# Kernel tuning notes

Hardware: AMD Instinct MI355X
Metric: run time of the kernel (lower is better)

Reference implementation:

```python
import jax, jax.numpy as jnp
import numpy as np

LN_EPS = 1e-6

def _log_g(x):
    return jnp.where(x >= 0, jnp.log(jax.nn.relu(x) + 0.5), -jax.nn.softplus(-x))

def setup_inputs() -> dict:
    key = jax.random.key(0)
    k1, k2 = jax.random.split(key)
    B, T, D = 8, 4096, 1024
    x = jax.random.normal(k1, (B, T, D), dtype=jnp.float32)
    W = jax.random.normal(k2, (D, 2 * D), dtype=jnp.float32) * (1.0 / np.sqrt(D))
    b = jnp.zeros((2 * D,), dtype=jnp.float32)
    gamma = jnp.ones((D,), dtype=jnp.float32)
    beta = jnp.zeros((D,), dtype=jnp.float32)
    return {"x": x, "W": W, "b": b, "gamma": gamma, "beta": beta}

def reference(x, W, b, gamma, beta):
    # projection: [B,T,D] @ [D,2D] -> [B,T,2D]
    projected = jnp.einsum('btd,de->bte', x, W) + b
    h_tilde, k = jnp.split(projected, 2, axis=-1)
    log_coeffs = -jax.nn.softplus(k)          # log(1-z)
    log_z = -jax.nn.softplus(-k)               # log(z)
    log_values = log_z + _log_g(h_tilde)
    # parallel scan in log space along time axis (-2)
    a_star = jnp.cumsum(log_coeffs, axis=-2)
    log_h0_plus_b_star = jax.lax.associative_scan(jnp.logaddexp, log_values - a_star, axis=-2)
    h = jnp.exp(a_star + log_h0_plus_b_star)
    # residual + LayerNorm (eps = flax nnx default 1e-6)
    y = x + h
    mu = jnp.mean(y, axis=-1, keepdims=True)
    var = jnp.mean(jnp.square(y - mu), axis=-1, keepdims=True)
    return (y - mu) * jax.lax.rsqrt(var + LN_EPS) * gamma + beta
```

## Files before the change

### kernel.cpp

```cpp
#include <hip/hip_runtime.h>
#include <hip/hip_bf16.h>

#define B_  8
#define T_  4096
#define D_  1024
#define M_  (B_*T_)
#define N_  (2*D_)
#define K_  D_
#define NC_ 32
#define C_  (T_/NC_)

typedef short bf16x8 __attribute__((ext_vector_type(8)));
typedef float f32x4  __attribute__((ext_vector_type(4)));

__device__ __forceinline__ unsigned short f2bf(float f) {
  union { float f; unsigned int u; } v; v.f = f;
  unsigned int r = (v.u + 0x7fffu + ((v.u >> 16) & 1u)) >> 16;
  return (unsigned short)r;
}

__device__ __forceinline__ float bf2f(unsigned short u) {
  union { unsigned int u; float f; } v; v.u = ((unsigned int)u) << 16; return v.f;
}

__device__ __forceinline__ float sigm(float x) {
  return 1.0f / (1.0f + __expf(-x));
}

__device__ __forceinline__ void async16(const void* g, void* l) {
  __builtin_amdgcn_global_load_lds((const __attribute__((address_space(1))) void*)g,
                                   (__attribute__((address_space(3))) void*)l,
                                   16, 0, 0);
}

__global__ void cast_x_kernel(const float* __restrict__ x, unsigned short* __restrict__ xb) {
  const long n4 = (long)M_ * K_ / 4;
  long i = (long)blockIdx.x * blockDim.x + threadIdx.x;
  const long stride = (long)gridDim.x * blockDim.x;
  for (; i < n4; i += stride) {
    float4 v = ((const float4*)x)[i];
    ushort4 o;
    o.x = f2bf(v.x); o.y = f2bf(v.y); o.z = f2bf(v.z); o.w = f2bf(v.w);
    ((ushort4*)xb)[i] = o;
  }
}

__global__ void cast_wt_kernel(const float* __restrict__ W, unsigned short* __restrict__ Wt) {
  __shared__ float tile[32][33];
  const int n0 = blockIdx.x * 32, k0 = blockIdx.y * 32;
  const int tx = threadIdx.x, ty = threadIdx.y;
  for (int i = 0; i < 32; i += 8)
    tile[ty + i][tx] = W[(size_t)(k0 + ty + i) * N_ + n0 + tx];
  __syncthreads();
  for (int i = 0; i < 32; i += 8)
    Wt[(size_t)(n0 + ty + i) * K_ + k0 + tx] = f2bf(tile[tx][ty + i]);
}

#define BM 128
#define BN 128
#define BK 64

__global__ __launch_bounds__(256, 3) void gemm_kernel(
    const unsigned short* __restrict__ A,
    const unsigned short* __restrict__ Bt,
    const float* __restrict__ bias,
    unsigned short* __restrict__ Sout,
    unsigned short* __restrict__ Gout) {
  __shared__ unsigned short lds[2 * BM * BK];
  unsigned short* As = lds;
  unsigned short* Bs = lds + BM * BK;

  const int tid  = threadIdx.x;
  const int wave = tid >> 6;
  const int lane = tid & 63;

  const int bid   = blockIdx.x;
  const int xcd   = bid & 7;
  const int j     = bid >> 3;
  const int n_idx = j & 15;
  const int m_idx = (j >> 4) * 8 + xcd;
  const int m0 = m_idx * BM;
  const int n0 = n_idx * BN;

  const int wm = wave >> 1;
  const int wn = wave & 1;
  const int n15  = lane & 15;
  const int quad = lane >> 4;

  f32x4 acc[4][4] = {};

  for (int k0 = 0; k0 < K_; k0 += BK) {
    for (int i = 0; i < 4; ++i) {
      const int seg = wave * 4 + i;
      const int row = seg * 8 + (lane >> 3);
      const int gg  = ((lane & 7) ^ (row & 7)) * 8;
      async16(A  + (size_t)(m0 + row) * K_ + k0 + gg, As + seg * 512);
      async16(Bt + (size_t)(n0 + row) * K_ + k0 + gg, Bs + seg * 512);
    }
    __syncthreads();

    for (int kk = 0; kk < 2; ++kk) {
      const int gg = kk * 4 + quad;
      bf16x8 af[4], bfr[4];
      for (int i = 0; i < 4; ++i) {
        const int row = wm * 64 + i * 16 + n15;
        af[i] = *(const bf16x8*)(As + (size_t)row * BK + ((gg ^ (row & 7)) * 8));
      }
      for (int jj = 0; jj < 4; ++jj) {
        const int row = wn * 64 + jj * 16 + n15;
        bfr[jj] = *(const bf16x8*)(Bs + (size_t)row * BK + ((gg ^ (row & 7)) * 8));
      }
      for (int i = 0; i < 4; ++i)
        for (int jj = 0; jj < 4; ++jj)
          acc[i][jj] = __builtin_amdgcn_mfma_f32_16x16x32_bf16(af[i], bfr[jj], acc[i][jj], 0, 0, 0);
    }
    __syncthreads();
  }

  const bool is_k = (n0 >= D_);
  unsigned short* __restrict__ dst = is_k ? Sout : Gout;
  for (int jj = 0; jj < 4; ++jj) {
    const int n = n0 + wn * 64 + jj * 16 + n15;
    const float bv = bias[n];
    const int d = is_k ? (n - D_) : n;
    for (int i = 0; i < 4; ++i) {
      const int mbase = m0 + wm * 64 + i * 16 + quad * 4;
      for (int r = 0; r < 4; ++r) {
        const float val = acc[i][jj][r] + bv;
        float o;
        if (is_k) o = sigm(val);
        else      o = (val >= 0.0f) ? (val + 0.5f) : sigm(val);
        dst[(size_t)(mbase + r) * D_ + d] = f2bf(o);
      }
    }
  }
}

__global__ void chunk_agg_kernel(const unsigned short* __restrict__ S,
                                 const unsigned short* __restrict__ G,
                                 float* __restrict__ AggA, float* __restrict__ AggV) {
  const int d = blockIdx.x * 256 + threadIdx.x;
  const int c = blockIdx.y;
  const int b = blockIdx.z;
  size_t base = ((size_t)b * T_ + (size_t)c * C_) * D_ + d;
  float Aa = 1.0f, V = 0.0f;
  for (int t = 0; t < C_; ++t) {
    const float s = bf2f(S[base]);
    const float g = bf2f(G[base]);
    const float a = 1.0f - s;
    V = fmaf(a, V, s * g);
    Aa *= a;
    base += D_;
  }
  const int idx = (b * NC_ + c) * D_ + d;
  AggA[idx] = Aa;
  AggV[idx] = V;
}

__global__ void chunk_scan_kernel(const float* __restrict__ AggA, const float* __restrict__ AggV,
                                  float* __restrict__ H0) {
  const int d = blockIdx.x * 256 + threadIdx.x;
  const int b = blockIdx.y;
  float h = 0.0f;
  for (int c = 0; c < NC_; ++c) {
    const int idx = (b * NC_ + c) * D_ + d;
    H0[idx] = h;
    h = fmaf(AggA[idx], h, AggV[idx]);
  }
}

__global__ __launch_bounds__(1024, 1) void scan_ln_kernel(
    const unsigned short* __restrict__ S, const unsigned short* __restrict__ G,
    const float* __restrict__ x, const float* __restrict__ H0,
    const float* __restrict__ gamma, const float* __restrict__ beta,
    float* __restrict__ out) {
  __shared__ float yb[16 * 1024];
  const int d = threadIdx.x;
  const int c = blockIdx.x;
  const int b = blockIdx.y;
  const int wid = d >> 6, lane = d & 63;

  float h = H0[(b * NC_ + c) * D_ + d];
  float gam[16], bet[16];
  for (int j = 0; j < 16; ++j) { gam[j] = gamma[lane + 64 * j]; bet[j] = beta[lane + 64 * j]; }

  size_t base = ((size_t)b * T_ + (size_t)c * C_) * D_ + d;
  for (int batch = 0; batch < 8; ++batch) {
    for (int tt = 0; tt < 16; ++tt) {
      const size_t idx = base + (size_t)tt * D_;
      const float s = bf2f(S[idx]);
      const float g = bf2f(G[idx]);
      h = fmaf(s, g - h, h);
      yb[tt * 1024 + d] = x[idx] + h;
    }
    __syncthreads();
    {
      float sy = 0.0f, sq = 0.0f;
      float yv[16];
      for (int j = 0; j < 16; ++j) {
        const float v = yb[wid * 1024 + lane + 64 * j];
        yv[j] = v; sy += v; sq += v * v;
      }
      for (int o = 32; o > 0; o >>= 1) {
        sy += __shfl_down(sy, o);
        sq += __shfl_down(sq, o);
      }
      sy = __shfl(sy, 0); sq = __shfl(sq, 0);
      const float mu   = sy * (1.0f / D_);
      const float rstd = rsqrtf(sq * (1.0f / D_) - mu * mu + 1e-6f);
      const size_t obase = ((size_t)b * T_ + (size_t)c * C_ + (size_t)batch * 16 + wid) * D_;
      for (int j = 0; j < 16; ++j)
        out[obase + lane + 64 * j] = (yv[j] - mu) * rstd * gam[j] + bet[j];
    }
    __syncthreads();
    base += (size_t)16 * D_;
  }
}

extern "C" void kernel_launch(void* const* d_in, const int* in_sizes, int n_in,
                              void* d_out, int out_size, void* d_ws, size_t ws_size,
                              hipStream_t stream) {
  const float* x     = (const float*)d_in[0];
  const float* W     = (const float*)d_in[1];
  const float* bias  = (const float*)d_in[2];
  const float* gamma = (const float*)d_in[3];
  const float* beta  = (const float*)d_in[4];
  float* out = (float*)d_out;

  char* ws = (char*)d_ws;
  unsigned short* Wt = (unsigned short*)ws;  ws += (size_t)N_ * K_ * 2;
  unsigned short* Xb = (unsigned short*)ws;  ws += (size_t)M_ * K_ * 2;
  unsigned short* S  = (unsigned short*)ws;  ws += (size_t)M_ * D_ * 2;
  unsigned short* G  = (unsigned short*)ws;  ws += (size_t)M_ * D_ * 2;
  float* AggA = (float*)ws;                  ws += (size_t)B_ * NC_ * D_ * 4;
  float* AggV = (float*)ws;                  ws += (size_t)B_ * NC_ * D_ * 4;
  float* H0   = (float*)ws;                  ws += (size_t)B_ * NC_ * D_ * 4;

  cast_x_kernel<<<4096, 256, 0, stream>>>(x, Xb);
  cast_wt_kernel<<<dim3(N_ / 32, K_ / 32), dim3(32, 8), 0, stream>>>(W, Wt);
  gemm_kernel<<<4096, 256, 0, stream>>>(Xb, Wt, bias, S, G);
  chunk_agg_kernel<<<dim3(D_ / 256, NC_, B_), 256, 0, stream>>>(S, G, AggA, AggV);
  chunk_scan_kernel<<<dim3(D_ / 256, B_), 256, 0, stream>>>(AggA, AggV, H0);
  scan_ln_kernel<<<dim3(NC_, B_), 1024, 0, stream>>>(S, G, x, H0, gamma, beta, out);
}
```

Measured before the change: 474.3 us.

## Rewrite GEMM as 256x256 double-buffered pipeline with LDS-staged coalesced epilogue

The projection GEMM moves from 128x128 tiles with a synchronous load-then-compute loop to 256x256 tiles on 512 threads. Global-to-LDS async loads for the next K tile are interleaved with MFMA phases using explicit barriers, waitcnt and setprio. The epilogue writes activated bf16 results into swizzled LDS and then stores them as coalesced 16-byte rows instead of scattered 2-byte stores. The larger tiles improve data reuse and the overlap hides load latency, at the cost of more registers and 128KB of LDS per block, which limits occupancy.

```diff
diff --git a/kernel.cpp b/kernel.cpp
--- a/kernel.cpp
+++ b/kernel.cpp
@@ -56,83 +56,166 @@
     Wt[(size_t)(n0 + ty + i) * K_ + k0 + tx] = f2bf(tile[tx][ty + i]);
 }
 
-#define BM 128
-#define BN 128
+#define BM 256
+#define BN 256
 #define BK 64
-
-__global__ __launch_bounds__(256, 3) void gemm_kernel(
+#define NT (K_/BK)
+#define LDSA(b) ((b)*32768)
+#define LDSB(b) ((b)*32768 + 16384)
+
+#define BARX()  __builtin_amdgcn_s_barrier()
+#define LGKM0() asm volatile("s_waitcnt lgkmcnt(0)" ::: "memory")
+#define SB0()   __builtin_amdgcn_sched_barrier(0)
+#define VM8()   asm volatile("s_waitcnt vmcnt(8)" ::: "memory")
+#define VM0()   asm volatile("s_waitcnt vmcnt(0)" ::: "memory")
+
+#define STAGE_Bt(BUF, KOFF) do {                                                \
+    _Pragma("unroll")                                                           \
+    for (int r = 0; r < 4; ++r)                                                 \
+      async16(aB + (KOFF) + r*64*K_, lds + LDSB(BUF) + w*512 + r*4096);         \
+  } while (0)
+#define STAGE_At(BUF, KOFF) do {                                                \
+    _Pragma("unroll")                                                           \
+    for (int r = 0; r < 4; ++r)                                                 \
+      async16(aA + (KOFF) + r*64*K_, lds + LDSA(BUF) + w*512 + r*4096);         \
+  } while (0)
+
+#define RD_A(MBASE, BUF) do {                                                   \
+    _Pragma("unroll")                                                           \
+    for (int m = 0; m < 4; ++m) {                                               \
+      af[m][0] = *(const bf16x8*)(lds + LDSA(BUF) + (rowA + (MBASE + m)*16)*64 + cc0); \
+      af[m][1] = *(const bf16x8*)(lds + LDSA(BUF) + (rowA + (MBASE + m)*16)*64 + cc1); \
+    } } while (0)
+#define RD_B(NBASE, BUF) do {                                                   \
+    _Pragma("unroll")                                                           \
+    for (int n = 0; n < 2; ++n) {                                               \
+      bfr[NBASE + n][0] = *(const bf16x8*)(lds + LDSB(BUF) + (rowB + (NBASE + n)*16)*64 + cc0); \
+      bfr[NBASE + n][1] = *(const bf16x8*)(lds + LDSB(BUF) + (rowB + (NBASE + n)*16)*64 + cc1); \
+    } } while (0)
+
+#define MFMA_Q(MB, NB) do {                                                     \
+    __builtin_amdgcn_s_setprio(1);                                              \
+    _Pragma("unroll")                                                           \
+    for (int m = 0; m < 4; ++m)                                                 \
+      _Pragma("unroll")                                                         \
+      for (int n = 0; n < 2; ++n) {                                             \
+        acc[MB+m][NB+n] = __builtin_amdgcn_mfma_f32_16x16x32_bf16(af[m][0], bfr[NB+n][0], acc[MB+m][NB+n], 0, 0, 0); \
+        acc[MB+m][NB+n] = __builtin_amdgcn_mfma_f32_16x16x32_bf16(af[m][1], bfr[NB+n][1], acc[MB+m][NB+n], 0, 0, 0); \
+      }                                                                         \
+    __builtin_amdgcn_s_setprio(0);                                              \
+  } while (0)
+
+#define TILE(BUF, DO_STAGE, KOFF, VMW) do {                                     \
+                                                                        \
+    RD_A(0, BUF); RD_B(0, BUF);                                                 \
+    BARX(); LGKM0(); SB0();                                                     \
+    MFMA_Q(0, 0);                                                               \
+    BARX();                                                                     \
+                                                                        \
+    RD_B(2, BUF);                                                               \
+    BARX(); LGKM0(); SB0();                                                     \
+    MFMA_Q(0, 2);                                                               \
+    BARX();                                                                     \
+                                                                        \
+    if (DO_STAGE) STAGE_Bt(BUF, KOFF);                                          \
+    RD_A(4, BUF);                                                               \
+    BARX(); LGKM0(); SB0();                                                     \
+    MFMA_Q(4, 0);                                                               \
+    BARX();                                                                     \
+                                                                        \
+    if (DO_STAGE) STAGE_At(BUF, KOFF);                                          \
+    MFMA_Q(4, 2);                                                               \
+    VMW;                                                                        \
+    BARX();                                                                     \
+  } while (0)
+
+__global__ __launch_bounds__(512, 2) void gemm_kernel(
     const unsigned short* __restrict__ A,
     const unsigned short* __restrict__ Bt,
     const float* __restrict__ bias,
     unsigned short* __restrict__ Sout,
     unsigned short* __restrict__ Gout) {
-  __shared__ unsigned short lds[2 * BM * BK];
-  unsigned short* As = lds;
-  unsigned short* Bs = lds + BM * BK;
+  __shared__ unsigned short lds[65536];
 
   const int tid  = threadIdx.x;
-  const int wave = tid >> 6;
+  const int w    = tid >> 6;
   const int lane = tid & 63;
+  const int wm   = w >> 2;
+  const int wn   = w & 3;
+  const int quad = lane >> 4, n15 = lane & 15;
 
   const int bid   = blockIdx.x;
   const int xcd   = bid & 7;
   const int j     = bid >> 3;
-  const int n_idx = j & 15;
-  const int m_idx = (j >> 4) * 8 + xcd;
-  const int m0 = m_idx * BM;
-  const int n0 = n_idx * BN;
-
-  const int wm = wave >> 1;
-  const int wn = wave & 1;
-  const int n15  = lane & 15;
-  const int quad = lane >> 4;
-
-  f32x4 acc[4][4] = {};
-
-  for (int k0 = 0; k0 < K_; k0 += BK) {
-    for (int i = 0; i < 4; ++i) {
-      const int seg = wave * 4 + i;
-      const int row = seg * 8 + (lane >> 3);
-      const int gg  = ((lane & 7) ^ (row & 7)) * 8;
-      async16(A  + (size_t)(m0 + row) * K_ + k0 + gg, As + seg * 512);
-      async16(Bt + (size_t)(n0 + row) * K_ + k0 + gg, Bs + seg * 512);
-    }
-    __syncthreads();
-
-    for (int kk = 0; kk < 2; ++kk) {
-      const int gg = kk * 4 + quad;
-      bf16x8 af[4], bfr[4];
-      for (int i = 0; i < 4; ++i) {
-        const int row = wm * 64 + i * 16 + n15;
-        af[i] = *(const bf16x8*)(As + (size_t)row * BK + ((gg ^ (row & 7)) * 8));
-      }
-      for (int jj = 0; jj < 4; ++jj) {
-        const int row = wn * 64 + jj * 16 + n15;
-        bfr[jj] = *(const bf16x8*)(Bs + (size_t)row * BK + ((gg ^ (row & 7)) * 8));
-      }
-      for (int i = 0; i < 4; ++i)
-        for (int jj = 0; jj < 4; ++jj)
-          acc[i][jj] = __builtin_amdgcn_mfma_f32_16x16x32_bf16(af[i], bfr[jj], acc[i][jj], 0, 0, 0);
-    }
-    __syncthreads();
-  }
+  const int n_idx = j & 7;
+  const int m_idx = (j >> 3) * 8 + xcd;
+  const int m0 = m_idx * BM, n0 = n_idx * BN;
+
+  const int lr = lane >> 3, lg = lane & 7;
+  const int sg8 = (lg ^ lr) * 8;
+  const unsigned short* aA = A  + (size_t)(m0 + w*8 + lr) * K_ + sg8;
+  const unsigned short* aB = Bt + (size_t)(n0 + w*8 + lr) * K_ + sg8;
+
+  const int n7  = n15 & 7;
+  const int cc0 = (quad ^ n7) * 8;
+  const int cc1 = cc0 ^ 32;
+  const int rowA = wm * 128 + n15;
+  const int rowB = wn * 64  + n15;
+
+  f32x4 acc[8][4];
+  #pragma unroll
+  for (int i = 0; i < 8; ++i)
+    #pragma unroll
+    for (int jj = 0; jj < 4; ++jj) acc[i][jj] = (f32x4){0.f, 0.f, 0.f, 0.f};
+
+  bf16x8 af[4][2], bfr[4][2];
+
+  STAGE_Bt(0, 0);  STAGE_At(0, 0);
+  STAGE_Bt(1, 64); STAGE_At(1, 64);
+  VM8();
+  BARX();
+
+  int koff = 128;
+  #pragma unroll 1
+  for (int it = 0; it < 7; ++it) {
+    TILE(0, 1, koff,      VM8());
+    TILE(1, 1, koff + 64, VM8());
+    koff += 128;
+  }
+  TILE(0, 0, 0, VM0());
+  TILE(1, 0, 0, ((void)0));
 
   const bool is_k = (n0 >= D_);
   unsigned short* __restrict__ dst = is_k ? Sout : Gout;
-  for (int jj = 0; jj < 4; ++jj) {
-    const int n = n0 + wn * 64 + jj * 16 + n15;
-    const float bv = bias[n];
-    const int d = is_k ? (n - D_) : n;
-    for (int i = 0; i < 4; ++i) {
-      const int mbase = m0 + wm * 64 + i * 16 + quad * 4;
+  const int d0 = is_k ? (n0 - D_) : n0;
+  float bv[4];
+  #pragma unroll
+  for (int jj = 0; jj < 4; ++jj) bv[jj] = bias[n0 + wn*64 + jj*16 + n15];
+
+  #pragma unroll
+  for (int i = 0; i < 8; ++i) {
+    #pragma unroll
+    for (int jj = 0; jj < 4; ++jj) {
+      const int col = wn*64 + jj*16 + n15;
+      #pragma unroll
       for (int r = 0; r < 4; ++r) {
-        const float val = acc[i][jj][r] + bv;
-        float o;
-        if (is_k) o = sigm(val);
-        else      o = (val >= 0.0f) ? (val + 0.5f) : sigm(val);
-        dst[(size_t)(mbase + r) * D_ + d] = f2bf(o);
+        const int row = wm*128 + i*16 + quad*4 + r;
+        const float val = acc[i][jj][r] + bv[jj];
+        const float o = is_k ? sigm(val)
+                             : ((val >= 0.0f) ? (val + 0.5f) : sigm(val));
+        const int slot = (col >> 3) ^ (row & 7);
+        lds[row*256 + slot*8 + (col & 7)] = f2bf(o);
       }
     }
+  }
+  __syncthreads();
+  const int trow = tid >> 5;
+  const int cg   = tid & 31;
+  #pragma unroll
+  for (int rr = 0; rr < 16; ++rr) {
+    const int row = rr*16 + trow;
+    const uint4 v = *(const uint4*)(lds + row*256 + ((cg ^ (row & 7)) * 8));
+    *(uint4*)(dst + (size_t)(m0 + row) * D_ + d0 + cg*8) = v;
   }
 }
 
@@ -238,7 +321,7 @@
 
   cast_x_kernel<<<4096, 256, 0, stream>>>(x, Xb);
   cast_wt_kernel<<<dim3(N_ / 32, K_ / 32), dim3(32, 8), 0, stream>>>(W, Wt);
-  gemm_kernel<<<4096, 256, 0, stream>>>(Xb, Wt, bias, S, G);
+  gemm_kernel<<<1024, 512, 0, stream>>>(Xb, Wt, bias, S, G);
   chunk_agg_kernel<<<dim3(D_ / 256, NC_, B_), 256, 0, stream>>>(S, G, AggA, AggV);
   chunk_scan_kernel<<<dim3(D_ / 256, B_), 256, 0, stream>>>(AggA, AggV, H0);
   scan_ln_kernel<<<dim3(NC_, B_), 1024, 0, stream>>>(S, G, x, H0, gamma, beta, out);
```

Result: no change. 477.1 us (+0.6%).
